# Optimization experiments

Hardware: AMD Instinct MI355X
Metric: run time of the kernel (lower is better)

## Reference

```python
import jax, jax.numpy as jnp
import numpy as np
from jax import lax

# Static model/config sizes
B, ANG, C, H, NF, NB = 1, 9, 3, 128, 16, 2


def get_freq_position(n):
    """Anti-diagonal frequency bands of an n x n angular-DCT grid (python/static)."""
    bands = []
    for i in range(n):
        bands.append(([i], [0]))
    for j in range(1, n):
        bands.append(([n - 1], [j]))
    for item in bands:
        while item[0][0] > 0 and item[1][0] < n - 1:
            item[0].insert(0, item[0][0] - 1)
            item[1].insert(0, item[1][0] + 1)
    return bands


def dct_mat(n):
    """Orthonormal DCT-II matrix (row k = k-th basis)."""
    k = jnp.arange(n, dtype=jnp.float32)[:, None]
    i = jnp.arange(n, dtype=jnp.float32)[None, :]
    m = jnp.cos(jnp.pi * (i + 0.5) * k / n) * jnp.sqrt(2.0 / n)
    return m.at[0].multiply(1.0 / np.sqrt(2.0))


def conv3d(x, w, b):
    # x: (N, Cin, D, H, W), w: (Cout, Cin, 3, 3, 3)
    y = lax.conv_general_dilated(x, w, (1, 1, 1), 'SAME',
                                 dimension_numbers=('NCDHW', 'OIDHW', 'NCDHW'))
    return y + b[None, :, None, None, None]


def branch(cut, wi, bi, a, wb, bb):
    """init conv + NB ResBlock3D (PReLU -> Conv3d, residual), plus outer skip."""
    y0 = conv3d(cut, wi, bi)
    y = y0
    for k in range(NB):
        r = jnp.where(y >= 0, y, a[k] * y)  # PReLU (single-parameter)
        y = y + conv3d(r, wb[k], bb[k])
    return y0 + y


def setup_inputs() -> dict:
    key = jax.random.key(0)
    ks = jax.random.split(key, 32)

    def nrm(k, shape, s=0.05):
        return jax.random.normal(k, shape, dtype=jnp.float32) * s

    inp = {"x": jax.random.normal(ks[0], (B, ANG, ANG, C, H, H), dtype=jnp.float32)}
    i = 1
    for n in ("dc", "lo", "mi", "hi"):
        inp[f"w_{n}_i"] = nrm(ks[i], (NF, C, 3, 3, 3)); i += 1
        inp[f"b_{n}_i"] = nrm(ks[i], (NF,)); i += 1
        inp[f"a_{n}"] = jnp.full((NB,), 0.25, dtype=jnp.float32)
        inp[f"w_{n}"] = nrm(ks[i], (NB, NF, NF, 3, 3, 3)); i += 1
        inp[f"b_{n}"] = nrm(ks[i], (NB, NF)); i += 1
    inp["w_last"] = nrm(ks[i], (C, NF))  # 1x1 Conv2d, no bias
    return inp


def reference(x, w_dc_i, b_dc_i, a_dc, w_dc, b_dc,
              w_lo_i, b_lo_i, a_lo, w_lo, b_lo,
              w_mi_i, b_mi_i, a_mi, w_mi, b_mi,
              w_hi_i, b_hi_i, a_hi, w_hi, b_hi, w_last):
    b, u, v, c, h, w = x.shape
    Da = dct_mat(u)  # angular DCT (u == v)
    Ds = dct_mat(h)  # spatial DCT (h == w)

    # SpaAngDCT: spatial 2D DCT then angular 2D DCT
    xf = jnp.einsum('buvchw,Hh,Ww->buvcHW', x, Ds, Ds)
    xf = jnp.einsum('buvchw,Uu,Vv->bUVchw', xf, Da, Da)

    x_rec = jnp.zeros((b, NF, u, v, h, w), dtype=x.dtype)
    for idx, (ui, vi) in enumerate(get_freq_position(u)):
        if idx == 0:
            p = (w_dc_i, b_dc_i, a_dc, w_dc, b_dc)
        elif idx <= 2:
            p = (w_lo_i, b_lo_i, a_lo, w_lo, b_lo)
        elif idx <= u - 1:
            p = (w_mi_i, b_mi_i, a_mi, w_mi, b_mi)
        else:
            p = (w_hi_i, b_hi_i, a_hi, w_hi, b_hi)
        ua, va = jnp.array(ui), jnp.array(vi)
        cut = xf[:, ua, va].transpose(0, 2, 1, 3, 4)  # (b, c, L, h, w)
        out = branch(cut, *p)                          # (b, NF, L, h, w)
        x_rec = x_rec.at[:, :, ua, va].set(out)        # scatter band back

    # 'b c u v h w -> b c (u h) (v w)' then 1x1 conv (NF -> 3)
    xr = x_rec.transpose(0, 1, 2, 4, 3, 5).reshape(b, NF, u * h, v * w)
    xr = jnp.einsum('bnHW,on->boHW', xr, w_last)
    xr = xr.reshape(b, c, u, h, v, w).transpose(0, 2, 4, 1, 3, 5)  # (b,u,v,c,h,w)

    # InverseSpaAngDCT: angular IDCT then spatial IDCT
    xr = jnp.einsum('bUVchw,Uu,Vv->buvchw', xr, Da, Da)
    xr = jnp.einsum('buvcHW,Hh,Ww->buvchw', xr, Ds, Ds)
    return xr + x
```

## Files before the change

### kernel.cpp

```cpp
#include <hip/hip_runtime.h>
#include <hip/hip_bf16.h>
#include <math.h>

typedef __hip_bfloat16 bf16;
typedef __attribute__((ext_vector_type(8))) short short8;
typedef __attribute__((ext_vector_type(4))) float floatx4;
typedef __attribute__((ext_vector_type(4))) unsigned int uint4v;
typedef __attribute__((ext_vector_type(2))) unsigned int uint2v;

#define HW 16384
#define NSLICE 243

__constant__ int c_s_of_p[81] = {
  0, 1,1, 2,2,2, 3,3,3,3, 4,4,4,4,4, 5,5,5,5,5,5, 6,6,6,6,6,6,6,
  7,7,7,7,7,7,7,7, 8,8,8,8,8,8,8,8,8, 9,9,9,9,9,9,9,9,
  10,10,10,10,10,10,10, 11,11,11,11,11,11, 12,12,12,12,12,
  13,13,13,13, 14,14,14, 15,15, 16};
__constant__ int c_l_of_p[81] = {
  0, 0,1, 0,1,2, 0,1,2,3, 0,1,2,3,4, 0,1,2,3,4,5, 0,1,2,3,4,5,6,
  0,1,2,3,4,5,6,7, 0,1,2,3,4,5,6,7,8, 0,1,2,3,4,5,6,7,
  0,1,2,3,4,5,6, 0,1,2,3,4,5, 0,1,2,3,4, 0,1,2,3, 0,1,2, 0,1, 0};
__constant__ int c_L_of_s[17] = {1,2,3,4,5,6,7,8,9,8,7,6,5,4,3,2,1};
__constant__ int c_g_of_s[17] = {0,1,1,2,2,2,2,2,2,3,3,3,3,3,3,3,3};
__constant__ int c_pos_uv[81] = {
  0,1,3,6,10,15,21,28,36,
  2,4,7,11,16,22,29,37,45,
  5,8,12,17,23,30,38,46,53,
  9,13,18,24,31,39,47,54,60,
  14,19,25,32,40,48,55,61,66,
  20,26,33,41,49,56,62,67,71,
  27,34,42,50,57,63,68,72,75,
  35,43,51,58,64,69,73,76,78,
  44,52,59,65,70,74,77,79,80};

struct WPtrs {
  const float* wi[4]; const float* bi[4]; const float* a[4];
  const float* wb[4]; const float* bb[4]; const float* wl;
};

__device__ __forceinline__ unsigned short f2bf(float f) {
  return __bfloat16_as_ushort(__float2bfloat16(f));
}
__device__ __forceinline__ float bf2f(unsigned short u) {
  return __uint_as_float(((unsigned int)u) << 16);
}
__device__ __forceinline__ float bflo(unsigned int w) {
  return __uint_as_float(w << 16);
}
__device__ __forceinline__ float bfhi(unsigned int w) {
  return __uint_as_float(w & 0xffff0000u);
}
__device__ __forceinline__ unsigned int pack2(float a, float b) {
  return (unsigned int)f2bf(a) | ((unsigned int)f2bf(b) << 16);
}
__device__ __forceinline__ float invprelu(float v, float invA) {
  return (v >= 0.f) ? v : v * invA;
}
__device__ __forceinline__ void bfsplit(float v, unsigned short& hi, unsigned short& lo) {
  unsigned int bits = __float_as_uint(v);
  hi = (unsigned short)(bits >> 16);
  lo = f2bf(v - __uint_as_float(bits & 0xffff0000u));
}
__device__ __forceinline__ void gl_lds16(const void* g, void* l) {
  __builtin_amdgcn_global_load_lds(
      (const __attribute__((address_space(1))) unsigned int*)g,
      (__attribute__((address_space(3))) unsigned int*)l, 16, 0, 0);
}
__device__ __forceinline__ int ldsoff(int plane, int col) {
  return plane * 2112 + ((plane & 3) << 5) + (col << 4);
}

__global__ __launch_bounds__(256) void k_init(WPtrs P, float* DaF,
                                              unsigned short* TFhi, unsigned short* TFlo,
                                              unsigned short* TIhi, unsigned short* TIlo,
                                              unsigned short* Wmf,
                                              float* BiF, float* BbF,
                                              float* AF, float* WlF) {
  const double PI = 3.14159265358979323846;
  int t = blockIdx.x * 256 + threadIdx.x;
  if (t < 81) {
    int U = t / 9, u = t % 9;
    double d = cos(PI * (u + 0.5) * U / 9.0) * sqrt(2.0 / 9.0);
    if (U == 0) d *= (1.0 / sqrt(2.0));
    DaF[t] = (float)d;
  }
  if (t < 16384) {
    int jj = t & 7, lane = (t >> 3) & 63, ks = (t >> 9) & 3, tile = t >> 11;
    int row = tile * 16 + (lane & 15);
    int colk = ks * 32 + (lane >> 4) * 8 + jj;
    double vF = cos(PI * (colk + 0.5) * row / 128.0) * sqrt(2.0 / 128.0);
    if (row == 0) vF *= (1.0 / sqrt(2.0));
    double vI = cos(PI * (row + 0.5) * colk / 128.0) * sqrt(2.0 / 128.0);
    if (colk == 0) vI *= (1.0 / sqrt(2.0));
    unsigned short h, l;
    bfsplit((float)vF, h, l); TFhi[t] = h; TFlo[t] = l;
    bfsplit((float)vI, h, l); TIhi[t] = h; TIlo[t] = l;
  }
  if (t < 92160) {
    int s = t / 7680, r = t % 7680;
    int step = r / 512, r2 = r % 512;
    int lane = r2 >> 3, j = r2 & 7;
    int d = step / 5, i = step % 5;
    int q = lane >> 4, m = lane & 15;
    int tl = 2 * i + (q >> 1);
    int cin = (q & 1) * 8 + j;
    float val = 0.f;
    if (tl <= 8) {
      int ky = tl / 3, kx = tl % 3;
      int tap = d * 9 + ky * 3 + kx;
      if (s < 4) {
        if (cin < 3) val = P.wi[s][(m * 3 + cin) * 27 + tap];
      } else {
        int g = (s - 4) >> 1, k = (s - 4) & 1;
        val = P.wb[g][((k * 16 + m) * 16 + cin) * 27 + tap];
      }
    }
    Wmf[t] = f2bf(val);
  }
  if (t < 64)  BiF[t] = P.bi[t / 16][t % 16];
  if (t < 128) BbF[t] = P.bb[t / 32][t % 32];
  if (t < 8)   AF[t]  = P.a[t / 2][t % 2];
  if (t < 48)  WlF[t] = P.wl[t];
}

__global__ __launch_bounds__(256) void k_dct2(const float* __restrict__ X,
                                              const unsigned short* __restrict__ tabhi,
                                              const unsigned short* __restrict__ tablo,
                                              const float* __restrict__ xres,
                                              float* __restrict__ Yf,
                                              unsigned short* __restrict__ Ybf) {
  __shared__ unsigned short sThi[128 * 136];
  __shared__ unsigned short sTlo[128 * 136];
  int s = blockIdx.x;
  int t = threadIdx.x;
  int lane = t & 63, wv = t >> 6;
  int q = lane >> 4, n16 = lane & 15;
  const float* Xs = X + (size_t)s * HW;

  floatx4 acc[2][8];
#pragma unroll
  for (int mt = 0; mt < 2; mt++)
#pragma unroll
    for (int nt = 0; nt < 8; nt++) acc[mt][nt] = (floatx4){0.f, 0.f, 0.f, 0.f};

#pragma unroll
  for (int ks = 0; ks < 4; ks++) {
    short8 ahi[2], alo[2];
#pragma unroll
    for (int mt = 0; mt < 2; mt++) {
      const float* xp = Xs + (wv * 32 + mt * 16 + n16) * 128 + ks * 32 + q * 8;
      float4 a = *(const float4*)xp;
      float4 b = *(const float4*)(xp + 4);
      union { short8 v; unsigned short u[8]; } H, L;
      float xv[8] = {a.x, a.y, a.z, a.w, b.x, b.y, b.z, b.w};
#pragma unroll
      for (int j = 0; j < 8; j++) bfsplit(xv[j], H.u[j], L.u[j]);
      ahi[mt] = H.v; alo[mt] = L.v;
    }
#pragma unroll
    for (int nt = 0; nt < 8; nt++) {
      int e = nt * 2048 + ks * 512 + lane * 8;
      short8 bh = *(const short8*)(tabhi + e);
      short8 bl = *(const short8*)(tablo + e);
#pragma unroll
      for (int mt = 0; mt < 2; mt++) {
        acc[mt][nt] = __builtin_amdgcn_mfma_f32_16x16x32_bf16(ahi[mt], bl, acc[mt][nt], 0, 0, 0);
        acc[mt][nt] = __builtin_amdgcn_mfma_f32_16x16x32_bf16(alo[mt], bh, acc[mt][nt], 0, 0, 0);
        acc[mt][nt] = __builtin_amdgcn_mfma_f32_16x16x32_bf16(ahi[mt], bh, acc[mt][nt], 0, 0, 0);
      }
    }
  }

#pragma unroll
  for (int mt = 0; mt < 2; mt++)
#pragma unroll
    for (int nt = 0; nt < 8; nt++) {
      int col = nt * 16 + n16;
      int rowb = wv * 32 + mt * 16 + q * 4;
#pragma unroll
      for (int rp = 0; rp < 4; rp += 2) {
        unsigned short h0, l0, h1, l1;
        bfsplit(acc[mt][nt][rp], h0, l0);
        bfsplit(acc[mt][nt][rp + 1], h1, l1);
        int widx = (col * 136 + rowb + rp) >> 1;
        ((unsigned int*)sThi)[widx] = (unsigned int)h0 | ((unsigned int)h1 << 16);
        ((unsigned int*)sTlo)[widx] = (unsigned int)l0 | ((unsigned int)l1 << 16);
      }
    }
  __syncthreads();

#pragma unroll
  for (int mt = 0; mt < 2; mt++)
#pragma unroll
    for (int nt = 0; nt < 8; nt++) acc[mt][nt] = (floatx4){0.f, 0.f, 0.f, 0.f};

#pragma unroll
  for (int ks = 0; ks < 4; ks++) {
    short8 ahi[2], alo[2];
#pragma unroll
    for (int mt = 0; mt < 2; mt++) {
      int e = (wv * 2 + mt) * 2048 + ks * 512 + lane * 8;
      ahi[mt] = *(const short8*)(tabhi + e);
      alo[mt] = *(const short8*)(tablo + e);
    }
#pragma unroll
    for (int nt = 0; nt < 8; nt++) {
      int off = (nt * 16 + n16) * 136 + ks * 32 + q * 8;
      short8 bh = *(const short8*)(sThi + off);
      short8 bl = *(const short8*)(sTlo + off);
#pragma unroll
      for (int mt = 0; mt < 2; mt++) {
        acc[mt][nt] = __builtin_amdgcn_mfma_f32_16x16x32_bf16(ahi[mt], bl, acc[mt][nt], 0, 0, 0);
        acc[mt][nt] = __builtin_amdgcn_mfma_f32_16x16x32_bf16(alo[mt], bh, acc[mt][nt], 0, 0, 0);
        acc[mt][nt] = __builtin_amdgcn_mfma_f32_16x16x32_bf16(ahi[mt], bh, acc[mt][nt], 0, 0, 0);
      }
    }
  }

#pragma unroll
  for (int mt = 0; mt < 2; mt++)
#pragma unroll
    for (int nt = 0; nt < 8; nt++) {
      int row0 = wv * 32 + mt * 16 + q * 4;
      int col = nt * 16 + n16;
#pragma unroll
      for (int r = 0; r < 4; r++) {
        size_t oi = (size_t)s * HW + (size_t)(row0 + r) * 128 + col;
        float v = acc[mt][nt][r];
        if (Ybf) {
          Ybf[oi] = f2bf(v);
        } else {
          if (xres) v += xres[oi];
          Yf[oi] = v;
        }
      }
    }
}

__global__ __launch_bounds__(256) void k_angu(const unsigned short* __restrict__ in,
                                              const float* __restrict__ DaF,
                                              unsigned short* __restrict__ out) {
  __shared__ float sDa[81];
  int t = threadIdx.x;
  if (t < 81) sDa[t] = DaF[t];
  __syncthreads();
  int idx = blockIdx.x * 256 + t;
  int hw = idx & (HW - 1);
  int r = idx >> 14;
  int c = r % 3, v = r / 3;
  float f[9];
#pragma unroll
  for (int u = 0; u < 9; u++) f[u] = bf2f(in[(size_t)((u * 9 + v) * 3 + c) * HW + hw]);
#pragma unroll
  for (int U = 0; U < 9; U++) {
    float acc = 0.f;
#pragma unroll
    for (int u = 0; u < 9; u++) acc += sDa[U * 9 + u] * f[u];
    out[(size_t)((U * 9 + v) * 3 + c) * HW + hw] = f2bf(acc);
  }
}

__global__ __launch_bounds__(256) void k_angv(const unsigned short* __restrict__ in,
                                              const float* __restrict__ DaF,
                                              unsigned short* __restrict__ xf2b) {
  __shared__ float sDa[81];
  int t = threadIdx.x;
  if (t < 81) sDa[t] = DaF[t];
  __syncthreads();
  int idx = blockIdx.x * 256 + t;
  int hw = idx & (HW - 1);
  int r = idx >> 14;
  int c = r % 3, U = r / 3;
  float f[9];
#pragma unroll
  for (int v = 0; v < 9; v++) f[v] = bf2f(in[(size_t)((U * 9 + v) * 3 + c) * HW + hw]);
#pragma unroll
  for (int V = 0; V < 9; V++) {
    float acc = 0.f;
#pragma unroll
    for (int v = 0; v < 9; v++) acc += sDa[V * 9 + v] * f[v];
    size_t base = ((size_t)c_pos_uv[U * 9 + V] * HW + hw) * 4;
    xf2b[base + c] = f2bf(acc);
    if (c == 0) xf2b[base + 3] = 0;
  }
}

__global__ __launch_bounds__(256) void k_angvi(const float* __restrict__ xrb,
                                               const float* __restrict__ DaF,
                                               unsigned short* __restrict__ out) {
  __shared__ float sDa[81];
  int t = threadIdx.x;
  if (t < 81) sDa[t] = DaF[t];
  __syncthreads();
  int idx = blockIdx.x * 256 + t;
  int hw = idx & (HW - 1);
  int r = idx >> 14;
  int c = r % 3, U = r / 3;
  float f[9];
#pragma unroll
  for (int V = 0; V < 9; V++)
    f[V] = xrb[((size_t)c_pos_uv[U * 9 + V] * 3 + c) * HW + hw];
#pragma unroll
  for (int v = 0; v < 9; v++) {
    float acc = 0.f;
#pragma unroll
    for (int V = 0; V < 9; V++) acc += sDa[V * 9 + v] * f[V];
    out[(size_t)((U * 9 + v) * 3 + c) * HW + hw] = f2bf(acc);
  }
}

__global__ __launch_bounds__(256) void k_angui(const unsigned short* __restrict__ in,
                                               const float* __restrict__ DaF,
                                               float* __restrict__ out) {
  __shared__ float sDa[81];
  int t = threadIdx.x;
  if (t < 81) sDa[t] = DaF[t];
  __syncthreads();
  int idx = blockIdx.x * 256 + t;
  int hw = idx & (HW - 1);
  int r = idx >> 14;
  int c = r % 3, v = r / 3;
  float f[9];
#pragma unroll
  for (int U = 0; U < 9; U++) f[U] = bf2f(in[(size_t)((U * 9 + v) * 3 + c) * HW + hw]);
#pragma unroll
  for (int u = 0; u < 9; u++) {
    float acc = 0.f;
#pragma unroll
    for (int U = 0; U < 9; U++) acc += sDa[U * 9 + u] * f[U];
    out[(size_t)((u * 9 + v) * 3 + c) * HW + hw] = acc;
  }
}

__global__ __launch_bounds__(512) void k_conv(const unsigned short* __restrict__ src,
                                              const unsigned short* __restrict__ prevAct,
                                              const unsigned short* __restrict__ act0,
                                              const unsigned short* __restrict__ Wmf,
                                              const float* __restrict__ BiF,
                                              const float* __restrict__ BbF,
                                              const float* __restrict__ AF,
                                              const float* __restrict__ WlF,
                                              int sel,
                                              unsigned short* __restrict__ boutAct,
                                              float* __restrict__ xrbOut) {
  __shared__ unsigned short s_lds[21184];
  int p = blockIdx.y;
  int s = c_s_of_p[p], l = c_l_of_p[p];
  int g = c_g_of_s[s], Ls = c_L_of_s[s];
  int row0 = blockIdx.x * 8;
  int t = threadIdx.x;
  int lane = t & 63, wv = t >> 6;
  int q = lane >> 4, n = lane & 15;

  float aNext = (sel < 2) ? AF[g * 2 + sel] : 0.f;
  float invA  = (sel > 0) ? 1.0f / AF[g * 2 + sel - 1] : 0.f;

  int scol = t & 127;
  int shalf = (t >> 7) & 1;
  int srow0 = t >> 8;

  {
    uint4v z = (uint4v){0u, 0u, 0u, 0u};
    int zmax = (sel == 0) ? 1320 : 40;
    for (int i = t; i < zmax; i += 512) {
      int row, half, col;
      if (i < 40) { row = i >> 2; half = (i >> 1) & 1; col = (i & 1) ? 129 : 0; }
      else { int j = i - 40; row = j >> 7; col = (j & 127) + 1; half = 1; }
      *(uint4v*)((char*)s_lds + ldsoff(row * 2 + half, col)) = z;
    }
    for (int row = 0; row < 10; row++) {
      int grow = row0 - 1 + row;
      if ((unsigned)grow >= 128u) {
        for (int i = t; i < 264; i += 512) {
          int half = i / 132, col = i % 132;
          *(uint4v*)((char*)s_lds + ldsoff(row * 2 + half, col)) = z;
        }
      }
    }
  }

  int off2[5];
#pragma unroll
  for (int i = 0; i < 5; i++) {
    int tl = 2 * i + (q >> 1);
    if (tl > 8) tl = 8;
    int ky = tl / 3, kx = tl % 3;
    off2[i] = ldsoff(2 * (wv + ky) + (q & 1), n + kx);
  }

  int setIdx = (sel == 0) ? g : (4 + g * 2 + (sel - 1));
  const char* WsetBase = (const char*)Wmf + (size_t)setIdx * 15 * 1024;

  floatx4 acc[8];
#pragma unroll
  for (int cg = 0; cg < 8; cg++) acc[cg] = (floatx4){0.f, 0.f, 0.f, 0.f};

  for (int d = 0; d < 3; d++) {
    int l2 = l + d - 1;
    if (l2 < 0 || l2 >= Ls) continue;
    int p2 = p + d - 1;
    __syncthreads();
    if (sel == 0) {
      if (shalf == 0) {
#pragma unroll
        for (int it = 0; it < 5; it++) {
          int row = srow0 + it * 2;
          int grow = row0 - 1 + row;
          if ((unsigned)grow < 128u) {
            uint2v v2 = *(const uint2v*)(src + ((size_t)p2 * HW + grow * 128 + scol) * 4);
            uint4v val; val.x = v2.x; val.y = v2.y; val.z = 0u; val.w = 0u;
            *(uint4v*)((char*)s_lds + ldsoff(row * 2, scol + 1)) = val;
          }
        }
      }
    } else {
#pragma unroll
      for (int it = 0; it < 5; it++) {
        int row = srow0 + it * 2;
        int grow = row0 - 1 + row;
        if ((unsigned)grow < 128u) {
          const void* gp = (const void*)(src +
              (((size_t)p2 * HW + (size_t)grow * 128 + scol) * 16 + shalf * 8));
          void* lp = (void*)((char*)s_lds +
              ldsoff(row * 2 + shalf, (wv & 1) * 64 + 1));
          gl_lds16(gp, lp);
        }
      }
    }
    __syncthreads();
    short8 af[5];
#pragma unroll
    for (int i = 0; i < 5; i++)
      af[i] = *(const short8*)(WsetBase + ((d * 5 + i) * 64 + lane) * 16);
#pragma unroll
    for (int cg = 0; cg < 8; cg++) {
#pragma unroll
      for (int i = 0; i < 5; i++) {
        short8 b = *(const short8*)((const char*)s_lds + off2[i] + cg * 256);
        acc[cg] = __builtin_amdgcn_mfma_f32_16x16x32_bf16(af[i], b, acc[cg], 0, 0, 0);
      }
    }
  }

  const float* bp = (sel == 0) ? (BiF + g * 16) : (BbF + g * 32 + (sel - 1) * 16);
  float bz[4];
#pragma unroll
  for (int r = 0; r < 4; r++) bz[r] = bp[q * 4 + r];
  int h = row0 + wv;

  if (sel < 2) {
#pragma unroll
    for (int cg = 0; cg < 8; cg++) {
      size_t pix = (size_t)p * HW + h * 128 + cg * 16 + n;
      float r0 = acc[cg][0] + bz[0], r1 = acc[cg][1] + bz[1];
      float r2 = acc[cg][2] + bz[2], r3 = acc[cg][3] + bz[3];
      if (sel != 0) {
        uint2v pv = *(const uint2v*)(prevAct + pix * 16 + q * 4);
        r0 += invprelu(bflo(pv.x), invA); r1 += invprelu(bfhi(pv.x), invA);
        r2 += invprelu(bflo(pv.y), invA); r3 += invprelu(bfhi(pv.y), invA);
      }
      r0 = fmaxf(r0, 0.f) + aNext * fminf(r0, 0.f);
      r1 = fmaxf(r1, 0.f) + aNext * fminf(r1, 0.f);
      r2 = fmaxf(r2, 0.f) + aNext * fminf(r2, 0.f);
      r3 = fmaxf(r3, 0.f) + aNext * fminf(r3, 0.f);
      uint2v ov; ov.x = pack2(r0, r1); ov.y = pack2(r2, r3);
      *(uint2v*)(boutAct + pix * 16 + q * 4) = ov;
    }
  } else {
    float invA0 = 1.0f / AF[g * 2];
    float wl0[4], wl1[4], wl2[4];
#pragma unroll
    for (int r = 0; r < 4; r++) {
      wl0[r] = WlF[q * 4 + r];
      wl1[r] = WlF[16 + q * 4 + r];
      wl2[r] = WlF[32 + q * 4 + r];
    }
#pragma unroll
    for (int cg = 0; cg < 8; cg++) {
      size_t pix = (size_t)p * HW + h * 128 + cg * 16 + n;
      float r0 = acc[cg][0] + bz[0], r1 = acc[cg][1] + bz[1];
      float r2 = acc[cg][2] + bz[2], r3 = acc[cg][3] + bz[3];
      uint2v pv = *(const uint2v*)(prevAct + pix * 16 + q * 4);
      r0 += invprelu(bflo(pv.x), invA); r1 += invprelu(bfhi(pv.x), invA);
      r2 += invprelu(bflo(pv.y), invA); r3 += invprelu(bfhi(pv.y), invA);
      uint2v p0 = *(const uint2v*)(act0 + pix * 16 + q * 4);
      r0 += invprelu(bflo(p0.x), invA0); r1 += invprelu(bfhi(p0.x), invA0);
      r2 += invprelu(bflo(p0.y), invA0); r3 += invprelu(bfhi(p0.y), invA0);
      float o0 = wl0[0] * r0 + wl0[1] * r1 + wl0[2] * r2 + wl0[3] * r3;
      float o1 = wl1[0] * r0 + wl1[1] * r1 + wl1[2] * r2 + wl1[3] * r3;
      float o2 = wl2[0] * r0 + wl2[1] * r1 + wl2[2] * r2 + wl2[3] * r3;
      o0 += __shfl_xor(o0, 16); o0 += __shfl_xor(o0, 32);
      o1 += __shfl_xor(o1, 16); o1 += __shfl_xor(o1, 32);
      o2 += __shfl_xor(o2, 16); o2 += __shfl_xor(o2, 32);
      if (q == 0) {
        size_t hw = (size_t)h * 128 + cg * 16 + n;
        xrbOut[((size_t)p * 3 + 0) * HW + hw] = o0;
        xrbOut[((size_t)p * 3 + 1) * HW + hw] = o1;
        xrbOut[((size_t)p * 3 + 2) * HW + hw] = o2;
      }
    }
  }
}

extern "C" void kernel_launch(void* const* d_in, const int* in_sizes, int n_in,
                              void* d_out, int out_size, void* d_ws, size_t ws_size,
                              hipStream_t stream) {
  (void)in_sizes; (void)n_in; (void)out_size; (void)ws_size;
  const float* x = (const float*)d_in[0];
  WPtrs P;
  for (int g = 0; g < 4; g++) {
    int b = 1 + g * 5;
    P.wi[g] = (const float*)d_in[b + 0];
    P.bi[g] = (const float*)d_in[b + 1];
    P.a[g]  = (const float*)d_in[b + 2];
    P.wb[g] = (const float*)d_in[b + 3];
    P.bb[g] = (const float*)d_in[b + 4];
  }
  P.wl = (const float*)d_in[21];

  char* base = (char*)d_ws;
  size_t off = 0;
  auto take = [&](size_t bytes) -> char* {
    char* r = base + off;
    off += (bytes + 255) & ~(size_t)255;
    return r;
  };
  float* DaF = (float*)take(81 * 4);
  unsigned short* TFhi = (unsigned short*)take(16384 * 2);
  unsigned short* TFlo = (unsigned short*)take(16384 * 2);
  unsigned short* TIhi = (unsigned short*)take(16384 * 2);
  unsigned short* TIlo = (unsigned short*)take(16384 * 2);
  unsigned short* Wmf = (unsigned short*)take(92160 * 2);
  float* BiF   = (float*)take(256);
  float* BbF   = (float*)take(512);
  float* AF    = (float*)take(32);
  float* WlF   = (float*)take(192);
  float* R1 = (float*)take((size_t)NSLICE * HW * 4);
  unsigned short* B1 = (unsigned short*)take((size_t)NSLICE * HW * 2);
  unsigned short* B2 = (unsigned short*)take((size_t)NSLICE * HW * 2);
  float* R3 = (float*)take((size_t)NSLICE * HW * 4);
  unsigned short* braw0 = (unsigned short*)take((size_t)81 * 16 * HW * 2);
  unsigned short* braw1 = (unsigned short*)take((size_t)81 * 16 * HW * 2);
  unsigned short* xf2b = (unsigned short*)R3;
  float* xrb = R3;

  k_init<<<360, 256, 0, stream>>>(P, DaF, TFhi, TFlo, TIhi, TIlo,
                                  Wmf, BiF, BbF, AF, WlF);
  k_dct2<<<243, 256, 0, stream>>>(x, TFhi, TFlo, nullptr, nullptr, B1);
  k_angu<<<1728, 256, 0, stream>>>(B1, DaF, B2);
  k_angv<<<1728, 256, 0, stream>>>(B2, DaF, xf2b);
  k_conv<<<dim3(16, 81), 512, 0, stream>>>(xf2b, nullptr, nullptr, Wmf,
                                           BiF, BbF, AF, WlF, 0, braw0, nullptr);
  k_conv<<<dim3(16, 81), 512, 0, stream>>>(braw0, braw0, nullptr, Wmf,
                                           BiF, BbF, AF, WlF, 1, braw1, nullptr);
  k_conv<<<dim3(16, 81), 512, 0, stream>>>(braw1, braw1, braw0, Wmf,
                                           BiF, BbF, AF, WlF, 2, nullptr, xrb);
  k_angvi<<<1728, 256, 0, stream>>>(xrb, DaF, B1);
  k_angui<<<1728, 256, 0, stream>>>(B1, DaF, R1);
  k_dct2<<<243, 256, 0, stream>>>(R1, TIhi, TIlo, x, (float*)d_out, nullptr);
}
```

Measured before the change: 288.7 us.

## Prefetch next depth slice into registers to overlap global loads with MFMA

Replaces the direct global-to-LDS loads with register staging. The next depth slice's tile is loaded into registers while the current slice's MFMAs run, then written to LDS after a barrier, so global latency overlaps compute. The zero-fill for out-of-range rows is folded into the staged values, and the LDS zeroing is trimmed to the halo columns and the unused half planes. The cost is more registers and hand-placed barriers and waitcnts that must keep the LDS reads and writes ordered correctly.

```diff
diff --git a/kernel.cpp b/kernel.cpp
--- a/kernel.cpp
+++ b/kernel.cpp
@@ -61,11 +61,6 @@
   hi = (unsigned short)(bits >> 16);
   lo = f2bf(v - __uint_as_float(bits & 0xffff0000u));
 }
-__device__ __forceinline__ void gl_lds16(const void* g, void* l) {
-  __builtin_amdgcn_global_load_lds(
-      (const __attribute__((address_space(1))) unsigned int*)g,
-      (__attribute__((address_space(3))) unsigned int*)l, 16, 0, 0);
-}
 __device__ __forceinline__ int ldsoff(int plane, int col) {
   return plane * 2112 + ((plane & 3) << 5) + (col << 4);
 }
@@ -359,26 +354,6 @@
   int shalf = (t >> 7) & 1;
   int srow0 = t >> 8;
 
-  {
-    uint4v z = (uint4v){0u, 0u, 0u, 0u};
-    int zmax = (sel == 0) ? 1320 : 40;
-    for (int i = t; i < zmax; i += 512) {
-      int row, half, col;
-      if (i < 40) { row = i >> 2; half = (i >> 1) & 1; col = (i & 1) ? 129 : 0; }
-      else { int j = i - 40; row = j >> 7; col = (j & 127) + 1; half = 1; }
-      *(uint4v*)((char*)s_lds + ldsoff(row * 2 + half, col)) = z;
-    }
-    for (int row = 0; row < 10; row++) {
-      int grow = row0 - 1 + row;
-      if ((unsigned)grow >= 128u) {
-        for (int i = t; i < 264; i += 512) {
-          int half = i / 132, col = i % 132;
-          *(uint4v*)((char*)s_lds + ldsoff(row * 2 + half, col)) = z;
-        }
-      }
-    }
-  }
-
   int off2[5];
 #pragma unroll
   for (int i = 0; i < 5; i++) {
@@ -391,47 +366,77 @@
   int setIdx = (sel == 0) ? g : (4 + g * 2 + (sel - 1));
   const char* WsetBase = (const char*)Wmf + (size_t)setIdx * 15 * 1024;
 
+  int dlo = (l == 0) ? 1 : 0;
+  int dhi = (Ls - l >= 2) ? 2 : 1;
+
+  uint4v st[5];
+  short8 af[5];
   floatx4 acc[8];
 #pragma unroll
   for (int cg = 0; cg < 8; cg++) acc[cg] = (floatx4){0.f, 0.f, 0.f, 0.f};
 
-  for (int d = 0; d < 3; d++) {
-    int l2 = l + d - 1;
-    if (l2 < 0 || l2 >= Ls) continue;
-    int p2 = p + d - 1;
-    __syncthreads();
+  auto stage_load = [&](int p2) {
+#pragma unroll
+    for (int it = 0; it < 5; it++) {
+      int row = srow0 + it * 2;
+      int grow = row0 - 1 + row;
+      uint4v v = (uint4v){0u, 0u, 0u, 0u};
+      if (sel == 0) {
+        if (shalf == 0 && (unsigned)grow < 128u) {
+          uint2v w = *(const uint2v*)(src +
+              ((size_t)p2 * HW + (size_t)grow * 128 + scol) * 4);
+          v.x = w.x; v.y = w.y;
+        }
+      } else {
+        if ((unsigned)grow < 128u)
+          v = *(const uint4v*)(src +
+              (((size_t)p2 * HW + (size_t)grow * 128 + scol) * 16 + shalf * 8));
+      }
+      st[it] = v;
+    }
+  };
+  auto stage_write = [&]() {
+#pragma unroll
+    for (int it = 0; it < 5; it++) {
+      int row = srow0 + it * 2;
+      if (sel == 0) {
+        if (shalf == 0)
+          *(uint4v*)((char*)s_lds + ldsoff(row * 2, scol + 1)) = st[it];
+      } else {
+        *(uint4v*)((char*)s_lds + ldsoff(row * 2 + shalf, scol + 1)) = st[it];
+      }
+    }
+  };
+
+  stage_load(p + dlo - 1);
+  {
+    uint4v z = (uint4v){0u, 0u, 0u, 0u};
+    for (int i = t; i < 40; i += 512) {
+      int row = i >> 2, half = (i >> 1) & 1, col = (i & 1) ? 129 : 0;
+      *(uint4v*)((char*)s_lds + ldsoff(row * 2 + half, col)) = z;
+    }
     if (sel == 0) {
-      if (shalf == 0) {
-#pragma unroll
-        for (int it = 0; it < 5; it++) {
-          int row = srow0 + it * 2;
-          int grow = row0 - 1 + row;
-          if ((unsigned)grow < 128u) {
-            uint2v v2 = *(const uint2v*)(src + ((size_t)p2 * HW + grow * 128 + scol) * 4);
-            uint4v val; val.x = v2.x; val.y = v2.y; val.z = 0u; val.w = 0u;
-            *(uint4v*)((char*)s_lds + ldsoff(row * 2, scol + 1)) = val;
-          }
-        }
-      }
-    } else {
-#pragma unroll
-      for (int it = 0; it < 5; it++) {
-        int row = srow0 + it * 2;
-        int grow = row0 - 1 + row;
-        if ((unsigned)grow < 128u) {
-          const void* gp = (const void*)(src +
-              (((size_t)p2 * HW + (size_t)grow * 128 + scol) * 16 + shalf * 8));
-          void* lp = (void*)((char*)s_lds +
-              ldsoff(row * 2 + shalf, (wv & 1) * 64 + 1));
-          gl_lds16(gp, lp);
-        }
-      }
-    }
-    __syncthreads();
-    short8 af[5];
+      for (int i = t; i < 1280; i += 512) {
+        int row = i >> 7, col = (i & 127) + 1;
+        *(uint4v*)((char*)s_lds + ldsoff(row * 2 + 1, col)) = z;
+      }
+    }
+  }
+
+  for (int d = dlo; d <= dhi; ++d) {
+    if (d > dlo) {
+      asm volatile("" ::: "memory");
+      __builtin_amdgcn_s_barrier();
+      asm volatile("" ::: "memory");
+    }
+    stage_write();
 #pragma unroll
     for (int i = 0; i < 5; i++)
       af[i] = *(const short8*)(WsetBase + ((d * 5 + i) * 64 + lane) * 16);
+    if (d < dhi) stage_load(p + d);
+    asm volatile("s_waitcnt lgkmcnt(0)" ::: "memory");
+    __builtin_amdgcn_s_barrier();
+    asm volatile("" ::: "memory");
 #pragma unroll
     for (int cg = 0; cg < 8; cg++) {
 #pragma unroll
```

Result: no change. 292.5 us (+1.3%).

## Fuse separable angular DCT passes and split conv tiles across 16 waves

Applied to the files above, without the earlier changes.

The two forward angular DCT kernels (u then v) are merged into one kernel, and likewise the two inverse ones. Each thread now keeps a 3x9 partial in registers, which removes the bf16 intermediate buffer round trip and two launches. The conv kernel moves from 512 to 1024 threads per block, with each wave covering half the columns (4 column groups instead of 8) and cooperative loads rebalanced to match. In exchange, the fused angular kernels launch only 576 blocks and use more registers per thread, and the conv kernel carries more threads per block under higher launch-bound pressure.

```diff
diff --git a/kernel.cpp b/kernel.cpp
--- a/kernel.cpp
+++ b/kernel.cpp
@@ -237,9 +237,9 @@
     }
 }
 
-__global__ __launch_bounds__(256) void k_angu(const unsigned short* __restrict__ in,
-                                              const float* __restrict__ DaF,
-                                              unsigned short* __restrict__ out) {
+__global__ __launch_bounds__(256) void k_angfwd(const unsigned short* __restrict__ in,
+                                                const float* __restrict__ DaF,
+                                                unsigned short* __restrict__ out) {
   __shared__ float sDa[81];
   int t = threadIdx.x;
   if (t < 81) sDa[t] = DaF[t];
@@ -247,22 +247,43 @@
   int idx = blockIdx.x * 256 + t;
   int hw = idx & (HW - 1);
   int r = idx >> 14;
-  int c = r % 3, v = r / 3;
-  float f[9];
-#pragma unroll
-  for (int u = 0; u < 9; u++) f[u] = bf2f(in[(size_t)((u * 9 + v) * 3 + c) * HW + hw]);
-#pragma unroll
-  for (int U = 0; U < 9; U++) {
-    float acc = 0.f;
-#pragma unroll
-    for (int u = 0; u < 9; u++) acc += sDa[U * 9 + u] * f[u];
-    out[(size_t)((U * 9 + v) * 3 + c) * HW + hw] = f2bf(acc);
-  }
-}
-
-__global__ __launch_bounds__(256) void k_angv(const unsigned short* __restrict__ in,
-                                              const float* __restrict__ DaF,
-                                              unsigned short* __restrict__ xf2b) {
+  int c = r % 3, ub = r / 3;
+  float tmp[3][9];
+#pragma unroll
+  for (int i = 0; i < 3; i++)
+#pragma unroll
+    for (int v = 0; v < 9; v++) tmp[i][v] = 0.f;
+#pragma unroll
+  for (int u = 0; u < 9; u++) {
+    float fv[9];
+#pragma unroll
+    for (int v = 0; v < 9; v++)
+      fv[v] = bf2f(in[(size_t)((u * 9 + v) * 3 + c) * HW + hw]);
+#pragma unroll
+    for (int i = 0; i < 3; i++) {
+      float dc = sDa[(ub * 3 + i) * 9 + u];
+#pragma unroll
+      for (int v = 0; v < 9; v++) tmp[i][v] += dc * fv[v];
+    }
+  }
+#pragma unroll
+  for (int i = 0; i < 3; i++) {
+    int U = ub * 3 + i;
+#pragma unroll
+    for (int V = 0; V < 9; V++) {
+      float acc = 0.f;
+#pragma unroll
+      for (int v = 0; v < 9; v++) acc += sDa[V * 9 + v] * tmp[i][v];
+      size_t base = ((size_t)c_pos_uv[U * 9 + V] * HW + hw) * 4;
+      out[base + c] = f2bf(acc);
+      if (c == 0) out[base + 3] = 0;
+    }
+  }
+}
+
+__global__ __launch_bounds__(256) void k_anginv(const float* __restrict__ xrb,
+                                                const float* __restrict__ DaF,
+                                                float* __restrict__ out) {
   __shared__ float sDa[81];
   int t = threadIdx.x;
   if (t < 81) sDa[t] = DaF[t];
@@ -270,69 +291,39 @@
   int idx = blockIdx.x * 256 + t;
   int hw = idx & (HW - 1);
   int r = idx >> 14;
-  int c = r % 3, U = r / 3;
-  float f[9];
-#pragma unroll
-  for (int v = 0; v < 9; v++) f[v] = bf2f(in[(size_t)((U * 9 + v) * 3 + c) * HW + hw]);
-#pragma unroll
-  for (int V = 0; V < 9; V++) {
-    float acc = 0.f;
-#pragma unroll
-    for (int v = 0; v < 9; v++) acc += sDa[V * 9 + v] * f[v];
-    size_t base = ((size_t)c_pos_uv[U * 9 + V] * HW + hw) * 4;
-    xf2b[base + c] = f2bf(acc);
-    if (c == 0) xf2b[base + 3] = 0;
-  }
-}
-
-__global__ __launch_bounds__(256) void k_angvi(const float* __restrict__ xrb,
-                                               const float* __restrict__ DaF,
-                                               unsigned short* __restrict__ out) {
-  __shared__ float sDa[81];
-  int t = threadIdx.x;
-  if (t < 81) sDa[t] = DaF[t];
-  __syncthreads();
-  int idx = blockIdx.x * 256 + t;
-  int hw = idx & (HW - 1);
-  int r = idx >> 14;
-  int c = r % 3, U = r / 3;
-  float f[9];
-#pragma unroll
-  for (int V = 0; V < 9; V++)
-    f[V] = xrb[((size_t)c_pos_uv[U * 9 + V] * 3 + c) * HW + hw];
-#pragma unroll
-  for (int v = 0; v < 9; v++) {
-    float acc = 0.f;
-#pragma unroll
-    for (int V = 0; V < 9; V++) acc += sDa[V * 9 + v] * f[V];
-    out[(size_t)((U * 9 + v) * 3 + c) * HW + hw] = f2bf(acc);
-  }
-}
-
-__global__ __launch_bounds__(256) void k_angui(const unsigned short* __restrict__ in,
-                                               const float* __restrict__ DaF,
-                                               float* __restrict__ out) {
-  __shared__ float sDa[81];
-  int t = threadIdx.x;
-  if (t < 81) sDa[t] = DaF[t];
-  __syncthreads();
-  int idx = blockIdx.x * 256 + t;
-  int hw = idx & (HW - 1);
-  int r = idx >> 14;
-  int c = r % 3, v = r / 3;
-  float f[9];
-#pragma unroll
-  for (int U = 0; U < 9; U++) f[U] = bf2f(in[(size_t)((U * 9 + v) * 3 + c) * HW + hw]);
-#pragma unroll
-  for (int u = 0; u < 9; u++) {
-    float acc = 0.f;
-#pragma unroll
-    for (int U = 0; U < 9; U++) acc += sDa[U * 9 + u] * f[U];
-    out[(size_t)((u * 9 + v) * 3 + c) * HW + hw] = acc;
-  }
-}
-
-__global__ __launch_bounds__(512) void k_conv(const unsigned short* __restrict__ src,
+  int c = r % 3, ub = r / 3;
+  float tmp[3][9];
+#pragma unroll
+  for (int i = 0; i < 3; i++)
+#pragma unroll
+    for (int V = 0; V < 9; V++) tmp[i][V] = 0.f;
+#pragma unroll
+  for (int U = 0; U < 9; U++) {
+    float fV[9];
+#pragma unroll
+    for (int V = 0; V < 9; V++)
+      fV[V] = xrb[((size_t)c_pos_uv[U * 9 + V] * 3 + c) * HW + hw];
+#pragma unroll
+    for (int i = 0; i < 3; i++) {
+      float dc = sDa[U * 9 + (ub * 3 + i)];
+#pragma unroll
+      for (int V = 0; V < 9; V++) tmp[i][V] += dc * fV[V];
+    }
+  }
+#pragma unroll
+  for (int i = 0; i < 3; i++) {
+    int u = ub * 3 + i;
+#pragma unroll
+    for (int v = 0; v < 9; v++) {
+      float acc = 0.f;
+#pragma unroll
+      for (int V = 0; V < 9; V++) acc += sDa[V * 9 + v] * tmp[i][V];
+      out[(size_t)((u * 9 + v) * 3 + c) * HW + hw] = acc;
+    }
+  }
+}
+
+__global__ __launch_bounds__(1024, 8) void k_conv(const unsigned short* __restrict__ src,
                                               const unsigned short* __restrict__ prevAct,
                                               const unsigned short* __restrict__ act0,
                                               const unsigned short* __restrict__ Wmf,
@@ -349,20 +340,17 @@
   int g = c_g_of_s[s], Ls = c_L_of_s[s];
   int row0 = blockIdx.x * 8;
   int t = threadIdx.x;
-  int lane = t & 63, wv = t >> 6;
+  int lane = t & 63, wv16 = t >> 6;
+  int row8 = wv16 & 7, ch = wv16 >> 3;
   int q = lane >> 4, n = lane & 15;
 
   float aNext = (sel < 2) ? AF[g * 2 + sel] : 0.f;
   float invA  = (sel > 0) ? 1.0f / AF[g * 2 + sel - 1] : 0.f;
-
-  int scol = t & 127;
-  int shalf = (t >> 7) & 1;
-  int srow0 = t >> 8;
 
   {
     uint4v z = (uint4v){0u, 0u, 0u, 0u};
     int zmax = (sel == 0) ? 1320 : 40;
-    for (int i = t; i < zmax; i += 512) {
+    for (int i = t; i < zmax; i += 1024) {
       int row, half, col;
       if (i < 40) { row = i >> 2; half = (i >> 1) & 1; col = (i & 1) ? 129 : 0; }
       else { int j = i - 40; row = j >> 7; col = (j & 127) + 1; half = 1; }
@@ -371,7 +359,7 @@
     for (int row = 0; row < 10; row++) {
       int grow = row0 - 1 + row;
       if ((unsigned)grow >= 128u) {
-        for (int i = t; i < 264; i += 512) {
+        for (int i = t; i < 264; i += 1024) {
           int half = i / 132, col = i % 132;
           *(uint4v*)((char*)s_lds + ldsoff(row * 2 + half, col)) = z;
         }
@@ -385,15 +373,15 @@
     int tl = 2 * i + (q >> 1);
     if (tl > 8) tl = 8;
     int ky = tl / 3, kx = tl % 3;
-    off2[i] = ldsoff(2 * (wv + ky) + (q & 1), n + kx);
+    off2[i] = ldsoff(2 * (row8 + ky) + (q & 1), n + kx) + ch * 1024;
   }
 
   int setIdx = (sel == 0) ? g : (4 + g * 2 + (sel - 1));
   const char* WsetBase = (const char*)Wmf + (size_t)setIdx * 15 * 1024;
 
-  floatx4 acc[8];
-#pragma unroll
-  for (int cg = 0; cg < 8; cg++) acc[cg] = (floatx4){0.f, 0.f, 0.f, 0.f};
+  floatx4 acc[4];
+#pragma unroll
+  for (int cg = 0; cg < 4; cg++) acc[cg] = (floatx4){0.f, 0.f, 0.f, 0.f};
 
   for (int d = 0; d < 3; d++) {
     int l2 = l + d - 1;
@@ -401,29 +389,33 @@
     int p2 = p + d - 1;
     __syncthreads();
     if (sel == 0) {
-      if (shalf == 0) {
-#pragma unroll
-        for (int it = 0; it < 5; it++) {
-          int row = srow0 + it * 2;
+#pragma unroll
+      for (int it = 0; it < 2; it++) {
+        int id = t + it * 1024;
+        if (id < 1280) {
+          int row = id >> 7, col = id & 127;
           int grow = row0 - 1 + row;
           if ((unsigned)grow < 128u) {
-            uint2v v2 = *(const uint2v*)(src + ((size_t)p2 * HW + grow * 128 + scol) * 4);
-            uint4v val; val.x = v2.x; val.y = v2.y; val.z = 0u; val.w = 0u;
-            *(uint4v*)((char*)s_lds + ldsoff(row * 2, scol + 1)) = val;
+            uint2v w = *(const uint2v*)(src +
+                ((size_t)p2 * HW + (size_t)grow * 128 + col) * 4);
+            uint4v val; val.x = w.x; val.y = w.y; val.z = 0u; val.w = 0u;
+            *(uint4v*)((char*)s_lds + ldsoff(row * 2, col + 1)) = val;
           }
         }
       }
     } else {
 #pragma unroll
-      for (int it = 0; it < 5; it++) {
-        int row = srow0 + it * 2;
-        int grow = row0 - 1 + row;
-        if ((unsigned)grow < 128u) {
-          const void* gp = (const void*)(src +
-              (((size_t)p2 * HW + (size_t)grow * 128 + scol) * 16 + shalf * 8));
-          void* lp = (void*)((char*)s_lds +
-              ldsoff(row * 2 + shalf, (wv & 1) * 64 + 1));
-          gl_lds16(gp, lp);
+      for (int it = 0; it < 3; it++) {
+        int id = t + it * 1024;
+        if (id < 2560) {
+          int row = id >> 8, half = (id >> 7) & 1, col = id & 127;
+          int grow = row0 - 1 + row;
+          if ((unsigned)grow < 128u) {
+            const void* gp = (const void*)(src +
+                (((size_t)p2 * HW + (size_t)grow * 128 + col) * 16 + half * 8));
+            void* lp = (void*)((char*)s_lds + ldsoff(row * 2 + half, col + 1));
+            gl_lds16(gp, lp);
+          }
         }
       }
     }
@@ -433,7 +425,7 @@
     for (int i = 0; i < 5; i++)
       af[i] = *(const short8*)(WsetBase + ((d * 5 + i) * 64 + lane) * 16);
 #pragma unroll
-    for (int cg = 0; cg < 8; cg++) {
+    for (int cg = 0; cg < 4; cg++) {
 #pragma unroll
       for (int i = 0; i < 5; i++) {
         short8 b = *(const short8*)((const char*)s_lds + off2[i] + cg * 256);
@@ -446,12 +438,12 @@
   float bz[4];
 #pragma unroll
   for (int r = 0; r < 4; r++) bz[r] = bp[q * 4 + r];
-  int h = row0 + wv;
+  int h = row0 + row8;
 
   if (sel < 2) {
 #pragma unroll
-    for (int cg = 0; cg < 8; cg++) {
-      size_t pix = (size_t)p * HW + h * 128 + cg * 16 + n;
+    for (int cg = 0; cg < 4; cg++) {
+      size_t pix = (size_t)p * HW + h * 128 + ch * 64 + cg * 16 + n;
       float r0 = acc[cg][0] + bz[0], r1 = acc[cg][1] + bz[1];
       float r2 = acc[cg][2] + bz[2], r3 = acc[cg][3] + bz[3];
       if (sel != 0) {
@@ -476,8 +468,8 @@
       wl2[r] = WlF[32 + q * 4 + r];
     }
 #pragma unroll
-    for (int cg = 0; cg < 8; cg++) {
-      size_t pix = (size_t)p * HW + h * 128 + cg * 16 + n;
+    for (int cg = 0; cg < 4; cg++) {
+      size_t pix = (size_t)p * HW + h * 128 + ch * 64 + cg * 16 + n;
       float r0 = acc[cg][0] + bz[0], r1 = acc[cg][1] + bz[1];
       float r2 = acc[cg][2] + bz[2], r3 = acc[cg][3] + bz[3];
       uint2v pv = *(const uint2v*)(prevAct + pix * 16 + q * 4);
@@ -493,7 +485,7 @@
       o1 += __shfl_xor(o1, 16); o1 += __shfl_xor(o1, 32);
       o2 += __shfl_xor(o2, 16); o2 += __shfl_xor(o2, 32);
       if (q == 0) {
-        size_t hw = (size_t)h * 128 + cg * 16 + n;
+        size_t hw = (size_t)h * 128 + ch * 64 + cg * 16 + n;
         xrbOut[((size_t)p * 3 + 0) * HW + hw] = o0;
         xrbOut[((size_t)p * 3 + 1) * HW + hw] = o1;
         xrbOut[((size_t)p * 3 + 2) * HW + hw] = o2;
@@ -537,7 +529,6 @@
   float* WlF   = (float*)take(192);
   float* R1 = (float*)take((size_t)NSLICE * HW * 4);
   unsigned short* B1 = (unsigned short*)take((size_t)NSLICE * HW * 2);
-  unsigned short* B2 = (unsigned short*)take((size_t)NSLICE * HW * 2);
   float* R3 = (float*)take((size_t)NSLICE * HW * 4);
   unsigned short* braw0 = (unsigned short*)take((size_t)81 * 16 * HW * 2);
   unsigned short* braw1 = (unsigned short*)take((size_t)81 * 16 * HW * 2);
@@ -547,15 +538,13 @@
   k_init<<<360, 256, 0, stream>>>(P, DaF, TFhi, TFlo, TIhi, TIlo,
                                   Wmf, BiF, BbF, AF, WlF);
   k_dct2<<<243, 256, 0, stream>>>(x, TFhi, TFlo, nullptr, nullptr, B1);
-  k_angu<<<1728, 256, 0, stream>>>(B1, DaF, B2);
-  k_angv<<<1728, 256, 0, stream>>>(B2, DaF, xf2b);
-  k_conv<<<dim3(16, 81), 512, 0, stream>>>(xf2b, nullptr, nullptr, Wmf,
-                                           BiF, BbF, AF, WlF, 0, braw0, nullptr);
-  k_conv<<<dim3(16, 81), 512, 0, stream>>>(braw0, braw0, nullptr, Wmf,
-                                           BiF, BbF, AF, WlF, 1, braw1, nullptr);
-  k_conv<<<dim3(16, 81), 512, 0, stream>>>(braw1, braw1, braw0, Wmf,
-                                           BiF, BbF, AF, WlF, 2, nullptr, xrb);
-  k_angvi<<<1728, 256, 0, stream>>>(xrb, DaF, B1);
-  k_angui<<<1728, 256, 0, stream>>>(B1, DaF, R1);
+  k_angfwd<<<576, 256, 0, stream>>>(B1, DaF, xf2b);
+  k_conv<<<dim3(16, 81), 1024, 0, stream>>>(xf2b, nullptr, nullptr, Wmf,
+                                            BiF, BbF, AF, WlF, 0, braw0, nullptr);
+  k_conv<<<dim3(16, 81), 1024, 0, stream>>>(braw0, braw0, nullptr, Wmf,
+                                            BiF, BbF, AF, WlF, 1, braw1, nullptr);
+  k_conv<<<dim3(16, 81), 1024, 0, stream>>>(braw1, braw1, braw0, Wmf,
+                                            BiF, BbF, AF, WlF, 2, nullptr, xrb);
+  k_anginv<<<576, 256, 0, stream>>>(xrb, DaF, R1);
   k_dct2<<<243, 256, 0, stream>>>(R1, TIhi, TIlo, x, (float*)d_out, nullptr);
 }
```

Result: faster. 278.6 us (-3.5%).
